# Kernel tuning notes

Measured on AMD Instinct MI355X. Metric: run time of the kernel, lower is better.

The kernel has to match this reference:

```python
import jax, jax.numpy as jnp
import numpy as np

N, E, D = 50000, 800000, 256   # nodes, edges, hidden_dim
H, B, A = 8, 4, 3              # num_heads, num_bases, num_aggregators (symnorm,sum,max)
F = D // H                      # per-head width = bases feature width
G = 64                          # number of graphs in the batch
EPS = 1e-5                      # GraphNorm eps


def setup_inputs() -> dict:
    key = jax.random.key(0)
    ks = jax.random.split(key, 8)
    glorot = lambda k, shape: jax.random.normal(k, shape, jnp.float32) * np.sqrt(2.0 / (shape[0] + shape[1])).astype(np.float32)
    return {
        "node": jax.random.normal(ks[0], (N, D), jnp.float32),
        "edge_attr": jax.random.normal(ks[1], (E, 1), jnp.float32),  # unused by layer, kept for signature fidelity
        "W_bases": glorot(ks[2], (D, B * F)),                 # EGConv bases linear (no bias)
        "W_comb": glorot(ks[3], (D, H * B * A)),              # EGConv combination-weight linear
        "b_comb": jnp.zeros((H * B * A,), jnp.float32),
        "conv_bias": jnp.zeros((D,), jnp.float32),
        "gn_weight": jnp.ones((D,), jnp.float32),             # GraphNorm gamma
        "gn_bias": jnp.zeros((D,), jnp.float32),              # GraphNorm beta
        "gn_mean_scale": jnp.ones((D,), jnp.float32),         # GraphNorm alpha
        "edge_index": jax.random.randint(ks[4], (2, E), 0, N, dtype=jnp.int32),
        "batch": jnp.sort(jax.random.randint(ks[5], (N,), 0, G, dtype=jnp.int32)),
    }


def _forward(node, W_bases, W_comb, b_comb, conv_bias, gn_weight, gn_bias, gn_mean_scale, edge_index, batch):
    n = node.shape[0]
    loops = jnp.arange(n, dtype=edge_index.dtype)
    src = jnp.concatenate([edge_index[0], loops])  # add self-loops (EGConv add_self_loops=True / gcn_norm)
    dst = jnp.concatenate([edge_index[1], loops])

    # gcn_norm symmetric weights deg^-1/2[src] * deg^-1/2[dst]
    deg = jax.ops.segment_sum(jnp.ones_like(src, dtype=node.dtype), dst, num_segments=n)
    dinv = jnp.where(deg > 0, jax.lax.rsqrt(deg), 0.0)
    sym_w = dinv[src] * dinv[dst]

    bases = node @ W_bases            # [N, B*F]
    comb = node @ W_comb + b_comb     # [N, H*B*A]

    msg = bases[src]                  # [E+N, B*F] edge gather (dominant traffic)
    agg_sym = jax.ops.segment_sum(msg * sym_w[:, None], dst, num_segments=n)
    agg_sum = jax.ops.segment_sum(msg, dst, num_segments=n)
    agg_max = jax.ops.segment_max(msg, dst, num_segments=n)  # self-loops guarantee non-empty segments

    aggregated = jnp.stack([agg_sym, agg_sum, agg_max], axis=1)       # [N, A, B*F]
    aggregated = aggregated.reshape(n, A * B, F)                      # (a,b) fused index, as in PyG view
    weightings = comb.reshape(n, H, B * A)
    h = jnp.einsum('nhk,nkf->nhf', weightings, aggregated).reshape(n, D) + conv_bias

    # GraphNorm: per-graph mean/var with learnable mean scale alpha
    counts = jnp.maximum(jax.ops.segment_sum(jnp.ones((n,), node.dtype), batch, num_segments=G), 1.0)
    mean = jax.ops.segment_sum(h, batch, num_segments=G) / counts[:, None]
    hc = h - gn_mean_scale * mean[batch]
    var = jax.ops.segment_sum(hc * hc, batch, num_segments=G) / counts[:, None]
    out = gn_weight * hc * jax.lax.rsqrt(var[batch] + EPS) + gn_bias
    return jax.nn.relu(out)


def reference(node, edge_attr, W_bases, W_comb, b_comb, conv_bias, gn_weight, gn_bias, gn_mean_scale, edge_index, batch):
    del edge_attr  # unused by EGConv_layer, present in the torch forward signature
    return _forward(node, W_bases, W_comb, b_comb, conv_bias, gn_weight, gn_bias, gn_mean_scale, edge_index, batch)
```

## Files before the change

### kernel.cpp

```cpp
#include <hip/hip_runtime.h>
#include <hip/hip_bf16.h>

#define NN 50000
#define EE 800000
#define DD 256
#define BF 128
#define HC 96
#define GG 64
#define NT 14
#define KCN 8
#define RC 98
#define RSH 9
#define RSZ 512
#define CC 256
#define CS 3125
#define CAP 10240
#define SL 16
#define STG 10752

typedef short s16x8 __attribute__((ext_vector_type(8)));
typedef float f32x4 __attribute__((ext_vector_type(4)));

static __device__ __forceinline__ float b2f(unsigned u) {
    unsigned x = u << 16;
    float f;
    __builtin_memcpy(&f, &x, 4);
    return f;
}
static __device__ __forceinline__ unsigned short f2b(float f) {
    unsigned x;
    __builtin_memcpy(&x, &f, 4);
    unsigned lsb = (x >> 16) & 1u;
    x += 0x7fffu + lsb;
    return (unsigned short)(x >> 16);
}
static __device__ __forceinline__ unsigned pack_trunc(float lo, float hi) {
    unsigned ulo, uhi;
    __builtin_memcpy(&ulo, &lo, 4);
    __builtin_memcpy(&uhi, &hi, 4);
    return (ulo >> 16) | (uhi & 0xffff0000u);
}

__global__ void k_setup(const unsigned short* node_u16, int* flag,
                        const void* bcomb, const void* cbias, const void* gw,
                        const void* gb, const void* gms,
                        float* bcombF, float* cbiasF, float* gwF, float* gbF, float* gmsF,
                        const int* batch, int* goff) {
    if (blockIdx.x == 0) {
        __shared__ int cnt;
        if (threadIdx.x == 0) cnt = 0;
        __syncthreads();
        int local = 0;
        #pragma unroll
        for (int j = 0; j < 4; j++) {
            int idx = 2 * (threadIdx.x * 4 + j);
            unsigned short u = node_u16[idx];
            int e = (u >> 7) & 0xFF;
            if (e < 100 || e > 140) local++;
        }
        atomicAdd(&cnt, local);
        __syncthreads();
        int isf = (cnt > 256) ? 1 : 0;
        if (threadIdx.x == 0) flag[0] = isf;
        int d = threadIdx.x;
        auto rd = [&](const void* p, int i) -> float {
            return isf ? ((const float*)p)[i] : b2f(((const unsigned short*)p)[i]);
        };
        if (d < HC) bcombF[d] = rd(bcomb, d);
        cbiasF[d] = rd(cbias, d);
        gwF[d] = rd(gw, d);
        gbF[d] = rd(gb, d);
        gmsF[d] = rd(gms, d);
    } else {
        int g = threadIdx.x;
        if (g > GG) return;
        int lo = 0, hi = NN;
        while (lo < hi) { int mid = (lo + hi) >> 1; if (batch[mid] < g) lo = mid + 1; else hi = mid; }
        goff[g] = lo;
    }
}

__global__ __launch_bounds__(256) void k_cnt(const int* ei, int* cntg) {
    __shared__ int cnt[RC];
    int c = blockIdx.x, t = threadIdx.x;
    if (t < RC) cnt[t] = 0;
    __syncthreads();
    const int* dstp = ei + EE + (size_t)c * CS;
    for (int i = t; i < CS; i += 256) atomicAdd(&cnt[dstp[i] >> RSH], 1);
    __syncthreads();
    if (t < RC) cntg[c * RC + t] = cnt[t];
}

__global__ __launch_bounds__(256) void k_cscan(const int* cntg, int* baseg, int* cntr) {
    __shared__ int lds[256];
    int r = blockIdx.x, t = threadIdx.x;
    int v = cntg[t * RC + r];
    lds[t] = v;
    __syncthreads();
    for (int ofs = 1; ofs < 256; ofs <<= 1) {
        int add = (t >= ofs) ? lds[t - ofs] : 0;
        __syncthreads();
        lds[t] += add;
        __syncthreads();
    }
    baseg[t * RC + r] = r * CAP + lds[t] - v;
    if (t == 255) cntr[r] = lds[255];
}

__global__ void k_rscan(const int* cntr, int* rbase, int* row_off) {
    __shared__ int lds[128];
    int t = threadIdx.x;
    int nr = (t < RC) ? ((t == RC - 1) ? (NN - (RC - 1) * RSZ) : RSZ) : 0;
    int v = (t < RC) ? cntr[t] + nr : 0;
    lds[t] = v;
    __syncthreads();
    for (int ofs = 1; ofs < 128; ofs <<= 1) {
        int add = (t >= ofs) ? lds[t - ofs] : 0;
        __syncthreads();
        lds[t] += add;
        __syncthreads();
    }
    if (t < RC) rbase[t] = lds[t] - v;
    if (t == RC - 1) row_off[NN] = lds[t];
}

__global__ __launch_bounds__(256) void k_bucket(const int* ei, const int* baseg, unsigned* bucket) {
    __shared__ int cur[RC];
    int c = blockIdx.x, t = threadIdx.x;
    if (t < RC) cur[t] = baseg[c * RC + t];
    __syncthreads();
    const int* srcp = ei + (size_t)c * CS;
    const int* dstp = ei + EE + (size_t)c * CS;
    for (int i = t; i < CS; i += 256) {
        int d = dstp[i], s = srcp[i];
        int r = d >> RSH;
        int pos = atomicAdd(&cur[r], 1);
        bucket[pos] = ((unsigned)s << RSH) | (unsigned)(d & (RSZ - 1));
    }
}

__global__ __launch_bounds__(256) void k_build(const unsigned* bucket, const int* cntr,
                                               const int* rbase, int* row_off, float* dinv,
                                               int* csr) {
    __shared__ int hist[RSZ];
    __shared__ int stage[STG];
    __shared__ int scanbuf[256];
    int r = blockIdx.x, t = threadIdx.x;
    int n0 = r * RSZ;
    int nr = NN - n0; if (nr > RSZ) nr = RSZ;
    int cr = cntr[r];
    int rb = rbase[r];
    const unsigned* bk = bucket + (size_t)r * CAP;
    #pragma unroll
    for (int j = 0; j < 2; j++) hist[t + j * 256] = 0;
    __syncthreads();
    for (int i = t; i < cr; i += 256) atomicAdd(&hist[bk[i] & (RSZ - 1)], 1);
    __syncthreads();
    int a0 = (2 * t     < nr) ? hist[2 * t] + 1     : 0;
    int a1 = (2 * t + 1 < nr) ? hist[2 * t + 1] + 1 : 0;
    int s = a0 + a1;
    scanbuf[t] = s;
    __syncthreads();
    for (int ofs = 1; ofs < 256; ofs <<= 1) {
        int add = (t >= ofs) ? scanbuf[t - ofs] : 0;
        __syncthreads();
        scanbuf[t] += add;
        __syncthreads();
    }
    int excl = scanbuf[t] - s;
    int total = scanbuf[255];
    __syncthreads();
    if (2 * t < nr) {
        int n = 2 * t;
        row_off[n0 + n] = rb + excl;
        dinv[n0 + n] = rsqrtf((float)a0);
        stage[excl] = n0 + n;
        hist[n] = excl + 1;
    }
    if (2 * t + 1 < nr) {
        int n = 2 * t + 1;
        int e1 = excl + a0;
        row_off[n0 + n] = rb + e1;
        dinv[n0 + n] = rsqrtf((float)a1);
        stage[e1] = n0 + n;
        hist[n] = e1 + 1;
    }
    __syncthreads();
    for (int i = t; i < cr; i += 256) {
        unsigned p = bk[i];
        int slot = atomicAdd(&hist[p & (RSZ - 1)], 1);
        stage[slot] = (int)(p >> RSH);
    }
    __syncthreads();
    for (int i = t; i < total; i += 256) csr[rb + i] = stage[i];
}

__global__ void k_pack(const int* flag, const void* Wb, const void* Wc, unsigned short* wpack) {
    int t = blockIdx.x, kc = blockIdx.y, lane = threadIdx.x;
    int isf = flag[0];
    int n = t * 16 + (lane & 15);
    int kb = kc * 32 + (lane >> 4) * 8;
    unsigned short* o = wpack + (size_t)(((t * KCN) + kc) * 64 + lane) * 8;
    #pragma unroll
    for (int j = 0; j < 8; j++) {
        int k = kb + j;
        int src = (n < BF) ? (k * BF + n) : (k * HC + (n - BF));
        const void* W = (n < BF) ? Wb : Wc;
        o[j] = isf ? f2b(((const float*)W)[src]) : ((const unsigned short*)W)[src];
    }
}

__global__ __launch_bounds__(128) void k_gemm(const int* flag, const void* node,
                                              const unsigned short* wpack, const float* bcombF,
                                              unsigned short* bases, float* comb) {
    int wv = threadIdx.x >> 6, lane = threadIdx.x & 63;
    int m = blockIdx.x * 16 + (lane & 15);
    int kg = lane >> 4;
    int isf = flag[0];
    const s16x8* bp = reinterpret_cast<const s16x8*>(wpack);
    f32x4 acc[7];
    #pragma unroll
    for (int t = 0; t < 7; t++) acc[t] = (f32x4){0.f, 0.f, 0.f, 0.f};
    if (isf) {
        const float* nf = (const float*)node + (size_t)m * DD;
        for (int kc = 0; kc < KCN; kc++) {
            const f32x4* src = reinterpret_cast<const f32x4*>(nf + kc * 32 + kg * 8);
            f32x4 x0 = src[0], x1 = src[1];
            union { s16x8 v; unsigned u[4]; } a;
            a.u[0] = pack_trunc(x0[0], x0[1]);
            a.u[1] = pack_trunc(x0[2], x0[3]);
            a.u[2] = pack_trunc(x1[0], x1[1]);
            a.u[3] = pack_trunc(x1[2], x1[3]);
            #pragma unroll
            for (int t2 = 0; t2 < 7; t2++) {
                int t = wv * 7 + t2;
                s16x8 b = bp[(size_t)(t * KCN + kc) * 64 + lane];
                acc[t2] = __builtin_amdgcn_mfma_f32_16x16x32_bf16(a.v, b, acc[t2], 0, 0, 0);
            }
        }
    } else {
        const s16x8* ap = reinterpret_cast<const s16x8*>(node);
        for (int kc = 0; kc < KCN; kc++) {
            s16x8 a = ap[(size_t)m * 32 + kc * 4 + kg];
            #pragma unroll
            for (int t2 = 0; t2 < 7; t2++) {
                int t = wv * 7 + t2;
                s16x8 b = bp[(size_t)(t * KCN + kc) * 64 + lane];
                acc[t2] = __builtin_amdgcn_mfma_f32_16x16x32_bf16(a, b, acc[t2], 0, 0, 0);
            }
        }
    }
    int colb = lane & 15;
    int row0 = blockIdx.x * 16;
    #pragma unroll
    for (int t2 = 0; t2 < 7; t2++) {
        int nc = (wv * 7 + t2) * 16 + colb;
        #pragma unroll
        for (int i = 0; i < 4; i++) {
            int r = row0 + kg * 4 + i;
            float v = acc[t2][i];
            if (nc < BF) bases[(size_t)r * BF + nc] = f2b(v);
            else comb[(size_t)r * HC + (nc - BF)] = v + bcombF[nc - BF];
        }
    }
}

__global__ __launch_bounds__(256) void k_agg(const unsigned short* bases,
                                             const float* comb, const float* dinv,
                                             const int* row_off, const int* csr,
                                             const float* cbiasF, unsigned short* h) {
    __shared__ float2 lds[4][3][64];
    int wv = threadIdx.x >> 6, lane = threadIdx.x & 63;
    int v = blockIdx.x * 4 + wv;
    int r0 = row_off[v], r1 = row_off[v + 1];
    float dv = dinv[v];
    const unsigned* bp = reinterpret_cast<const unsigned*>(bases);
    float sy0 = 0.f, sy1 = 0.f, su0 = 0.f, su1 = 0.f;
    float mx0 = -3.4e38f, mx1 = -3.4e38f;
    for (int base = r0; base < r1; base += 64) {
        int nload = r1 - base; if (nload > 64) nload = 64;
        int sidx = 0; float wgt = 0.f;
        if (lane < nload) { sidx = csr[base + lane]; wgt = dinv[sidx] * dv; }
        int j = 0;
        for (; j + 8 <= nload; j += 8) {
            int ss[8]; float ww[8]; unsigned gg[8];
            #pragma unroll
            for (int k = 0; k < 8; k++) { ss[k] = __shfl(sidx, j + k); ww[k] = __shfl(wgt, j + k); }
            #pragma unroll
            for (int k = 0; k < 8; k++) gg[k] = bp[(size_t)ss[k] * 64 + lane];
            #pragma unroll
            for (int k = 0; k < 8; k++) {
                float a = b2f(gg[k] & 0xffffu), b = b2f(gg[k] >> 16);
                sy0 += ww[k] * a; sy1 += ww[k] * b;
                su0 += a; su1 += b;
                mx0 = fmaxf(mx0, a); mx1 = fmaxf(mx1, b);
            }
        }
        for (; j < nload; j++) {
            int s0 = __shfl(sidx, j); float w0 = __shfl(wgt, j);
            unsigned g0 = bp[(size_t)s0 * 64 + lane];
            float a = b2f(g0 & 0xffffu), b = b2f(g0 >> 16);
            sy0 += w0 * a; sy1 += w0 * b; su0 += a; su1 += b; mx0 = fmaxf(mx0, a); mx1 = fmaxf(mx1, b);
        }
    }
    lds[wv][0][lane] = (float2){sy0, sy1};
    lds[wv][1][lane] = (float2){su0, su1};
    lds[wv][2][lane] = (float2){mx0, mx1};
    __syncthreads();
    const float* P0 = (const float*)&lds[wv][0][0];
    const float* P1 = (const float*)&lds[wv][1][0];
    const float* P2 = (const float*)&lds[wv][2][0];
    int d0 = lane * 4;
    int hh = d0 >> 5;
    float cb[12];
    #pragma unroll
    for (int k = 0; k < 12; k++) cb[k] = comb[(size_t)v * HC + hh * 12 + k];
    union { unsigned short e[4]; uint2 u; } o;
    #pragma unroll
    for (int i = 0; i < 4; i++) {
        int d = d0 + i, f = d & 31;
        float acc = cbiasF[d];
        #pragma unroll
        for (int k = 0; k < 12; k++) {
            int a = k >> 2, b = k & 3;
            const float* P = (a == 0) ? P0 : ((a == 1) ? P1 : P2);
            acc += cb[k] * P[b * 32 + f];
        }
        o.e[i] = f2b(acc);
    }
    reinterpret_cast<uint2*>(h)[(size_t)v * 64 + lane] = o.u;
}

__global__ __launch_bounds__(128) void k_stats1(const unsigned short* h, const int* goff, float* sstat) {
    int g = blockIdx.x, s = blockIdx.y, t = threadIdx.x;
    int v0 = goff[g], v1 = goff[g + 1];
    const unsigned* hu = reinterpret_cast<const unsigned*>(h);
    float s0 = 0.f, s1 = 0.f, q0 = 0.f, q1 = 0.f;
    for (int v = v0 + s; v < v1; v += SL) {
        unsigned x = hu[(size_t)v * 128 + t];
        float a = b2f(x & 0xffffu), b = b2f(x >> 16);
        s0 += a; s1 += b; q0 += a * a; q1 += b * b;
    }
    size_t o = ((size_t)(g * SL + s)) * (2 * DD);
    sstat[o + 2 * t] = s0;
    sstat[o + 2 * t + 1] = s1;
    sstat[o + DD + 2 * t] = q0;
    sstat[o + DD + 2 * t + 1] = q1;
}

__global__ void k_stats2(const float* sstat, const int* goff,
                         const float* gwF, const float* gbF, const float* gmsF,
                         float* sA, float* sB) {
    int g = blockIdx.x, d = threadIdx.x;
    float sum = 0.f, sq = 0.f;
    for (int s = 0; s < SL; s++) {
        size_t o = ((size_t)(g * SL + s)) * (2 * DD);
        sum += sstat[o + d];
        sq  += sstat[o + DD + d];
    }
    int c = goff[g + 1] - goff[g];
    float cnt = (float)(c > 1 ? c : 1);
    float mu = sum / cnt;
    float m2 = sq / cnt;
    float al = gmsF[d];
    float var = m2 - mu * mu * (2.f * al - al * al);
    float rstd = rsqrtf(var + 1e-5f);
    float sa = gwF[d] * rstd;
    sA[g * DD + d] = sa;
    sB[g * DD + d] = gbF[d] - sa * al * mu;
}

__global__ void k_out(const int* flag, const unsigned short* h, const int* batch,
                      const float* sA, const float* sB, void* out) {
    int tid = blockIdx.x * 256 + threadIdx.x;
    int v = tid >> 6, q = tid & 63;
    if (v >= NN) return;
    int g = batch[v];
    uint2 xr = reinterpret_cast<const uint2*>(h)[(size_t)v * 64 + q];
    f32x4 a = reinterpret_cast<const f32x4*>(sA)[g * 64 + q];
    f32x4 b = reinterpret_cast<const f32x4*>(sB)[g * 64 + q];
    float x0 = b2f(xr.x & 0xffffu), x1 = b2f(xr.x >> 16);
    float x2 = b2f(xr.y & 0xffffu), x3 = b2f(xr.y >> 16);
    float y0 = fmaxf(x0 * a[0] + b[0], 0.f);
    float y1 = fmaxf(x1 * a[1] + b[1], 0.f);
    float y2 = fmaxf(x2 * a[2] + b[2], 0.f);
    float y3 = fmaxf(x3 * a[3] + b[3], 0.f);
    if (flag[0]) {
        f32x4 y = {y0, y1, y2, y3};
        reinterpret_cast<f32x4*>(out)[(size_t)v * 64 + q] = y;
    } else {
        union { unsigned short e[4]; uint2 u; } o;
        o.e[0] = f2b(y0); o.e[1] = f2b(y1); o.e[2] = f2b(y2); o.e[3] = f2b(y3);
        reinterpret_cast<uint2*>(out)[(size_t)v * 64 + q] = o.u;
    }
}

extern "C" void kernel_launch(void* const* d_in, const int* in_sizes, int n_in,
                              void* d_out, int out_size, void* d_ws, size_t ws_size,
                              hipStream_t stream) {
    const void* node  = d_in[0];
    const void* Wb    = d_in[2];
    const void* Wc    = d_in[3];
    const void* bcomb = d_in[4];
    const void* cbias = d_in[5];
    const void* gw    = d_in[6];
    const void* gb    = d_in[7];
    const void* gms   = d_in[8];
    const int* ei     = (const int*)d_in[9];
    const int* batch  = (const int*)d_in[10];

    char* w = (char*)d_ws;
    size_t off = 0;
    auto alloc = [&](size_t bytes) -> void* {
        off = (off + 255) & ~(size_t)255;
        void* p = w + off;
        off += bytes;
        return p;
    };
    unsigned short* bases = (unsigned short*)alloc((size_t)NN * BF * 2);
    float* comb    = (float*)alloc((size_t)NN * HC * 4);
    unsigned short* h = (unsigned short*)alloc((size_t)NN * DD * 2);
    int*   csr     = (int*)alloc((size_t)(EE + NN) * 4);
    unsigned* bucket = (unsigned*)alloc((size_t)RC * CAP * 4);
    int*   cntg    = (int*)alloc((size_t)CC * RC * 4);
    int*   baseg   = (int*)alloc((size_t)CC * RC * 4);
    int*   cntrr   = (int*)alloc((size_t)RC * 4);
    int*   rbase   = (int*)alloc((size_t)RC * 4);
    float* dinv    = (float*)alloc((size_t)NN * 4);
    int*   row_off = (int*)alloc((size_t)(NN + 1) * 4);
    int*   goff    = (int*)alloc((size_t)(GG + 1) * 4);
    float* sstat   = (float*)alloc((size_t)GG * SL * 2 * DD * 4);
    float* sA      = (float*)alloc((size_t)GG * DD * 4);
    float* sB      = (float*)alloc((size_t)GG * DD * 4);
    unsigned short* wpack = (unsigned short*)alloc((size_t)NT * KCN * 64 * 8 * 2);
    int*   flag    = (int*)alloc(256);
    float* bcombF  = (float*)alloc(HC * 4);
    float* cbiasF  = (float*)alloc(DD * 4);
    float* gwF     = (float*)alloc(DD * 4);
    float* gbF     = (float*)alloc(DD * 4);
    float* gmsF    = (float*)alloc(DD * 4);

    k_setup<<<2, 256, 0, stream>>>((const unsigned short*)node, flag, bcomb, cbias, gw, gb, gms,
                                   bcombF, cbiasF, gwF, gbF, gmsF, batch, goff);
    k_cnt<<<CC, 256, 0, stream>>>(ei, cntg);
    k_cscan<<<RC, 256, 0, stream>>>(cntg, baseg, cntrr);
    k_rscan<<<1, 128, 0, stream>>>(cntrr, rbase, row_off);
    k_bucket<<<CC, 256, 0, stream>>>(ei, baseg, bucket);
    k_build<<<RC, 256, 0, stream>>>(bucket, cntrr, rbase, row_off, dinv, csr);
    k_pack<<<dim3(NT, KCN), 64, 0, stream>>>(flag, Wb, Wc, wpack);
    k_gemm<<<NN / 16, 128, 0, stream>>>(flag, node, wpack, bcombF, bases, comb);
    k_agg<<<NN / 4, 256, 0, stream>>>(bases, comb, dinv, row_off, csr, cbiasF, h);
    k_stats1<<<dim3(GG, SL), 128, 0, stream>>>(h, goff, sstat);
    k_stats2<<<GG, 256, 0, stream>>>(sstat, goff, gwF, gbF, gmsF, sA, sB);
    k_out<<<(NN * 64 + 255) / 256, 256, 0, stream>>>(flag, h, batch, sA, sB, d_out);
}
```

Before: 267.9 us.

## Retile GEMM to 64-row blocks with register reuse and store comb as bf16

The GEMM kernel now computes 64 rows per 256-thread block. Each wave covers 32 rows and 7 column tiles, so every weight fragment it loads feeds two MFMAs instead of one, which cuts repeated weight loads and raises MFMA work per load. The combination weights are also written as bf16 instead of fp32, halving the comb write and the later read in the aggregation kernel. The bf16 comb adds rounding error to the per-node mixing weights, and the larger tile raises register pressure.

Measured after the change: 269.0 us. About the same (+0.4%).

```diff
diff --git a/kernel.cpp b/kernel.cpp
--- a/kernel.cpp
+++ b/kernel.cpp
@@ -210,63 +210,74 @@
     }
 }
 
-__global__ __launch_bounds__(128) void k_gemm(const int* flag, const void* node,
+__global__ __launch_bounds__(256) void k_gemm(const int* flag, const void* node,
                                               const unsigned short* wpack, const float* bcombF,
-                                              unsigned short* bases, float* comb) {
+                                              unsigned short* bases, unsigned short* comb) {
     int wv = threadIdx.x >> 6, lane = threadIdx.x & 63;
-    int m = blockIdx.x * 16 + (lane & 15);
-    int kg = lane >> 4;
+    int colh = wv >> 1, rowh = wv & 1;
+    int kg = lane >> 4, colb = lane & 15;
+    int row0 = blockIdx.x * 64 + rowh * 32;
+    int nt0 = colh * 7;
     int isf = flag[0];
     const s16x8* bp = reinterpret_cast<const s16x8*>(wpack);
-    f32x4 acc[7];
-    #pragma unroll
-    for (int t = 0; t < 7; t++) acc[t] = (f32x4){0.f, 0.f, 0.f, 0.f};
-    if (isf) {
-        const float* nf = (const float*)node + (size_t)m * DD;
-        for (int kc = 0; kc < KCN; kc++) {
-            const f32x4* src = reinterpret_cast<const f32x4*>(nf + kc * 32 + kg * 8);
-            f32x4 x0 = src[0], x1 = src[1];
-            union { s16x8 v; unsigned u[4]; } a;
-            a.u[0] = pack_trunc(x0[0], x0[1]);
-            a.u[1] = pack_trunc(x0[2], x0[3]);
-            a.u[2] = pack_trunc(x1[0], x1[1]);
-            a.u[3] = pack_trunc(x1[2], x1[3]);
-            #pragma unroll
-            for (int t2 = 0; t2 < 7; t2++) {
-                int t = wv * 7 + t2;
-                s16x8 b = bp[(size_t)(t * KCN + kc) * 64 + lane];
-                acc[t2] = __builtin_amdgcn_mfma_f32_16x16x32_bf16(a.v, b, acc[t2], 0, 0, 0);
+    f32x4 acc[2][7];
+    #pragma unroll
+    for (int rg = 0; rg < 2; rg++)
+        #pragma unroll
+        for (int t = 0; t < 7; t++) acc[rg][t] = (f32x4){0.f, 0.f, 0.f, 0.f};
+    for (int kc = 0; kc < KCN; kc++) {
+        s16x8 b[7];
+        #pragma unroll
+        for (int t2 = 0; t2 < 7; t2++)
+            b[t2] = bp[(size_t)((nt0 + t2) * KCN + kc) * 64 + lane];
+        union { s16x8 v; unsigned u[4]; } a[2];
+        if (isf) {
+            #pragma unroll
+            for (int rg = 0; rg < 2; rg++) {
+                int m = row0 + rg * 16 + colb;
+                int mc = m < NN ? m : NN - 1;
+                const f32x4* src = reinterpret_cast<const f32x4*>(
+                    (const float*)node + (size_t)mc * DD + kc * 32 + kg * 8);
+                f32x4 x0 = src[0], x1 = src[1];
+                a[rg].u[0] = pack_trunc(x0[0], x0[1]);
+                a[rg].u[1] = pack_trunc(x0[2], x0[3]);
+                a[rg].u[2] = pack_trunc(x1[0], x1[1]);
+                a[rg].u[3] = pack_trunc(x1[2], x1[3]);
             }
-        }
-    } else {
-        const s16x8* ap = reinterpret_cast<const s16x8*>(node);
-        for (int kc = 0; kc < KCN; kc++) {
-            s16x8 a = ap[(size_t)m * 32 + kc * 4 + kg];
-            #pragma unroll
-            for (int t2 = 0; t2 < 7; t2++) {
-                int t = wv * 7 + t2;
-                s16x8 b = bp[(size_t)(t * KCN + kc) * 64 + lane];
-                acc[t2] = __builtin_amdgcn_mfma_f32_16x16x32_bf16(a, b, acc[t2], 0, 0, 0);
+        } else {
+            #pragma unroll
+            for (int rg = 0; rg < 2; rg++) {
+                int m = row0 + rg * 16 + colb;
+                int mc = m < NN ? m : NN - 1;
+                a[rg].v = reinterpret_cast<const s16x8*>(node)[(size_t)mc * 32 + kc * 4 + kg];
             }
         }
-    }
-    int colb = lane & 15;
-    int row0 = blockIdx.x * 16;
-    #pragma unroll
-    for (int t2 = 0; t2 < 7; t2++) {
-        int nc = (wv * 7 + t2) * 16 + colb;
-        #pragma unroll
-        for (int i = 0; i < 4; i++) {
-            int r = row0 + kg * 4 + i;
-            float v = acc[t2][i];
-            if (nc < BF) bases[(size_t)r * BF + nc] = f2b(v);
-            else comb[(size_t)r * HC + (nc - BF)] = v + bcombF[nc - BF];
+        #pragma unroll
+        for (int rg = 0; rg < 2; rg++)
+            #pragma unroll
+            for (int t2 = 0; t2 < 7; t2++)
+                acc[rg][t2] = __builtin_amdgcn_mfma_f32_16x16x32_bf16(a[rg].v, b[t2], acc[rg][t2], 0, 0, 0);
+    }
+    #pragma unroll
+    for (int rg = 0; rg < 2; rg++) {
+        #pragma unroll
+        for (int t2 = 0; t2 < 7; t2++) {
+            int nc = (nt0 + t2) * 16 + colb;
+            #pragma unroll
+            for (int i = 0; i < 4; i++) {
+                int r = row0 + rg * 16 + kg * 4 + i;
+                if (r < NN) {
+                    float v = acc[rg][t2][i];
+                    if (nc < BF) bases[(size_t)r * BF + nc] = f2b(v);
+                    else comb[(size_t)r * HC + (nc - BF)] = f2b(v + bcombF[nc - BF]);
+                }
+            }
         }
     }
 }
 
 __global__ __launch_bounds__(256) void k_agg(const unsigned short* bases,
-                                             const float* comb, const float* dinv,
+                                             const unsigned short* comb, const float* dinv,
                                              const int* row_off, const int* csr,
                                              const float* cbiasF, unsigned short* h) {
     __shared__ float2 lds[4][3][64];
@@ -314,7 +325,7 @@
     int hh = d0 >> 5;
     float cb[12];
     #pragma unroll
-    for (int k = 0; k < 12; k++) cb[k] = comb[(size_t)v * HC + hh * 12 + k];
+    for (int k = 0; k < 12; k++) cb[k] = b2f(comb[(size_t)v * HC + hh * 12 + k]);
     union { unsigned short e[4]; uint2 u; } o;
     #pragma unroll
     for (int i = 0; i < 4; i++) {
@@ -418,7 +429,7 @@
         return p;
     };
     unsigned short* bases = (unsigned short*)alloc((size_t)NN * BF * 2);
-    float* comb    = (float*)alloc((size_t)NN * HC * 4);
+    unsigned short* comb  = (unsigned short*)alloc((size_t)NN * HC * 2);
     unsigned short* h = (unsigned short*)alloc((size_t)NN * DD * 2);
     int*   csr     = (int*)alloc((size_t)(EE + NN) * 4);
     unsigned* bucket = (unsigned*)alloc((size_t)RC * CAP * 4);
@@ -448,7 +459,7 @@
     k_bucket<<<CC, 256, 0, stream>>>(ei, baseg, bucket);
     k_build<<<RC, 256, 0, stream>>>(bucket, cntrr, rbase, row_off, dinv, csr);
     k_pack<<<dim3(NT, KCN), 64, 0, stream>>>(flag, Wb, Wc, wpack);
-    k_gemm<<<NN / 16, 128, 0, stream>>>(flag, node, wpack, bcombF, bases, comb);
+    k_gemm<<<(NN + 63) / 64, 256, 0, stream>>>(flag, node, wpack, bcombF, bases, comb);
     k_agg<<<NN / 4, 256, 0, stream>>>(bases, comb, dinv, row_off, csr, cbiasF, h);
     k_stats1<<<dim3(GG, SL), 128, 0, stream>>>(h, goff, sstat);
     k_stats2<<<GG, 256, 0, stream>>>(sstat, goff, gwF, gbF, gmsF, sA, sB);
```
